# Kernel optimization log

Measured on AMD Instinct MI355X. Metric: run time of the kernel, lower is better.

## Reference

```python
import jax, jax.numpy as jnp
import numpy as np

D = 1024
H = 16
T_BLOCK = 2048


def setup_inputs() -> dict:
    key = jax.random.key(0)
    ks = jax.random.split(key, 12)
    B, T = 2, 2048
    s = lambda k, shape: jax.random.normal(k, shape, jnp.float32) * 0.02
    return {
        "x": jax.random.normal(ks[0], (B, T, D), jnp.float32),
        # layernorms
        "ln1_g": jnp.ones((D,), jnp.float32), "ln1_b": jnp.zeros((D,), jnp.float32),
        "ln2_g": jnp.ones((D,), jnp.float32), "ln2_b": jnp.zeros((D,), jnp.float32),
        # attention qkv projection ([in,out] layout) and output proj
        "w_qkv": s(ks[1], (D, 3 * D)), "b_qkv": jnp.zeros((3 * D,), jnp.float32),
        "w_o": s(ks[2], (D, D)), "b_o": jnp.zeros((D,), jnp.float32),
        # MLP
        "w_fc1": s(ks[3], (D, 4 * D)), "b_fc1": jnp.zeros((4 * D,), jnp.float32),
        "w_fc2": s(ks[4], (4 * D, D)), "b_fc2": jnp.zeros((D,), jnp.float32),
    }


def _layernorm(x, g, b, eps=1e-5):
    mu = jnp.mean(x, axis=-1, keepdims=True)
    var = jnp.var(x, axis=-1, keepdims=True)
    return (x - mu) * jax.lax.rsqrt(var + eps) * g + b


def _attention(x, w_qkv, b_qkv, w_o, b_o):
    B, T, C = x.shape
    hd = C // H
    qkv = x @ w_qkv + b_qkv                      # [B,T,3C]
    q, k, v = jnp.split(qkv, 3, axis=-1)
    split = lambda t: t.reshape(B, T, H, hd).transpose(0, 2, 1, 3)  # [B,H,T,hd]
    q, k, v = split(q), split(k), split(v)
    att = jnp.einsum("bhqd,bhkd->bhqk", q, k) / jnp.sqrt(jnp.float32(hd))
    causal = jnp.tril(jnp.ones((T, T), bool))
    att = jnp.where(causal[None, None], att, -jnp.inf)
    att = jax.nn.softmax(att, axis=-1)
    y = jnp.einsum("bhqk,bhkd->bhqd", att, v)    # [B,H,T,hd]
    y = y.transpose(0, 2, 1, 3).reshape(B, T, C)
    return y @ w_o + b_o


def reference(x, ln1_g, ln1_b, ln2_g, ln2_b, w_qkv, b_qkv, w_o, b_o,
              w_fc1, b_fc1, w_fc2, b_fc2):
    # dropout is identity in eval mode
    x = x + _attention(_layernorm(x, ln1_g, ln1_b), w_qkv, b_qkv, w_o, b_o)
    h = jax.nn.gelu(_layernorm(x, ln2_g, ln2_b) @ w_fc1 + b_fc1)
    return x + (h @ w_fc2 + b_fc2)
```

## Files before the change

kernel.cpp:

```cpp
#include <hip/hip_runtime.h>
#include <hip/hip_bf16.h>


using bf16 = __bf16;
using bf16x8 = __attribute__((ext_vector_type(8))) __bf16;
using floatx4 = __attribute__((ext_vector_type(4))) float;

#define D_ 1024
#define T_ 2048
#define B_ 2
#define H_ 16

static __device__ __forceinline__ bf16 f2bf(float f) { return (bf16)f; }

static __device__ __forceinline__ void async16(const void* g, void* l) {
  __builtin_amdgcn_global_load_lds(
      (const __attribute__((address_space(1))) void*)g,
      (__attribute__((address_space(3))) void*)l, 16, 0, 0);
}

static __device__ __forceinline__ float gelu_f(float v) {
  const float u2 = 1.5957691216057308f * (v + 0.044715f * v * v * v);
  return v / (1.0f + __expf(-u2));
}

__global__ void transpose_cast(const float* __restrict__ in, bf16* __restrict__ out,
                               int K, int N) {
  __shared__ float tile[32][33];
  const int n0 = blockIdx.x * 32, k0 = blockIdx.y * 32;
  const int tx = threadIdx.x, ty = threadIdx.y;
  for (int i = 0; i < 32; i += 8)
    tile[ty + i][tx] = in[(size_t)(k0 + ty + i) * N + n0 + tx];
  __syncthreads();
  for (int i = 0; i < 32; i += 8)
    out[(size_t)(n0 + ty + i) * K + k0 + tx] = f2bf(tile[tx][ty + i]);
}

__global__ __launch_bounds__(256)
void ln_kernel(const float* __restrict__ x, const float* __restrict__ g,
               const float* __restrict__ bsh, bf16* __restrict__ out) {
  const int row = blockIdx.x, tid = threadIdx.x;
  const float4 v = ((const float4*)(x + (size_t)row * D_))[tid];
  float s = v.x + v.y + v.z + v.w;
  float s2 = v.x * v.x + v.y * v.y + v.z * v.z + v.w * v.w;
  for (int off = 32; off; off >>= 1) {
    s += __shfl_xor(s, off);
    s2 += __shfl_xor(s2, off);
  }
  __shared__ float red[8];
  const int wave = tid >> 6, lane = tid & 63;
  if (lane == 0) { red[wave] = s; red[wave + 4] = s2; }
  __syncthreads();
  s = red[0] + red[1] + red[2] + red[3];
  s2 = red[4] + red[5] + red[6] + red[7];
  const float mu = s * (1.0f / D_);
  const float rstd = rsqrtf(s2 * (1.0f / D_) - mu * mu + 1e-5f);
  const float4 gv = ((const float4*)g)[tid];
  const float4 bv = ((const float4*)bsh)[tid];
  bf16 o[4] __attribute__((aligned(8)));
  o[0] = f2bf((v.x - mu) * rstd * gv.x + bv.x);
  o[1] = f2bf((v.y - mu) * rstd * gv.y + bv.y);
  o[2] = f2bf((v.z - mu) * rstd * gv.z + bv.z);
  o[3] = f2bf((v.w - mu) * rstd * gv.w + bv.w);
  *(ushort4*)(out + (size_t)row * D_ + tid * 4) = *(const ushort4*)o;
}

template <int EPI>
__global__ __launch_bounds__(256)
void gemm_bt(const bf16* __restrict__ A, const bf16* __restrict__ Bt,
             const float* __restrict__ bias, const float* __restrict__ res,
             void* __restrict__ Cout, int M, int N, int K) {
  __shared__ __align__(16) bf16 As[128][64];
  __shared__ __align__(16) bf16 Bs[128][64];
  const int tid = threadIdx.x;
  const int wave = tid >> 6, lane = tid & 63;
  const int quad = lane >> 4, l16 = lane & 15;
  const int wr = wave >> 1, wc = wave & 1;
  const int bm = blockIdx.x * 128, bn = blockIdx.y * 128;
  const int lrow8 = lane >> 3;
  const int lcol = (((lane & 7) ^ lrow8) * 8);

  floatx4 acc[4][4] = {};

  for (int k0 = 0; k0 < K; k0 += 64) {
    __syncthreads();
    for (int c = 0; c < 4; c++) {
      const int r = wave * 32 + c * 8;
      async16(&A[(size_t)(bm + r + lrow8) * K + k0 + lcol], &As[r][0]);
      async16(&Bt[(size_t)(bn + r + lrow8) * K + k0 + lcol], &Bs[r][0]);
    }
    __syncthreads();
    for (int ks = 0; ks < 2; ks++) {
      const int fc = ((quad + ks * 4) ^ (l16 & 7)) * 8;
      bf16x8 af[4], bfr[4];
      for (int mt = 0; mt < 4; mt++)
        af[mt] = *(const bf16x8*)&As[wr * 64 + mt * 16 + l16][fc];
      for (int nt = 0; nt < 4; nt++)
        bfr[nt] = *(const bf16x8*)&Bs[wc * 64 + nt * 16 + l16][fc];
      for (int mt = 0; mt < 4; mt++)
        for (int nt = 0; nt < 4; nt++)
          acc[mt][nt] = __builtin_amdgcn_mfma_f32_16x16x32_bf16(
              af[mt], bfr[nt], acc[mt][nt], 0, 0, 0);
    }
  }

  for (int mt = 0; mt < 4; mt++) {
    for (int nt = 0; nt < 4; nt++) {
      const int col = bn + wc * 64 + nt * 16 + l16;
      const float bcol = bias[col];
      for (int i = 0; i < 4; i++) {
        const int row = bm + wr * 64 + mt * 16 + quad * 4 + i;
        float v = acc[mt][nt][i] + bcol;
        if (EPI == 0) {
          ((bf16*)Cout)[(size_t)row * N + col] = f2bf(v);
        } else if (EPI == 1) {
          ((bf16*)Cout)[(size_t)row * N + col] = f2bf(gelu_f(v));
        } else {
          ((float*)Cout)[(size_t)row * N + col] = v + res[(size_t)row * N + col];
        }
      }
    }
  }
}

template <int EPI>
__global__ __launch_bounds__(256)
void gemm64_k64(const bf16* __restrict__ A, const bf16* __restrict__ Bt,
                const float* __restrict__ bias, const float* __restrict__ res,
                void* __restrict__ Cout, int M, int N, int K) {
  __shared__ __align__(16) bf16 As[64][64];
  __shared__ __align__(16) bf16 Bs[128][64];
  const int tid = threadIdx.x;
  const int wave = tid >> 6, lane = tid & 63;
  const int quad = lane >> 4, l16 = lane & 15;
  const int wr = wave >> 1, wc = wave & 1;
  const int bm = blockIdx.x * 64, bn = blockIdx.y * 128;
  const int lrow8 = lane >> 3;
  const int lcol = (((lane & 7) ^ lrow8) * 8);

  floatx4 acc[2][4] = {};

  for (int k0 = 0; k0 < K; k0 += 64) {
    __syncthreads();
    for (int c = 0; c < 2; c++) {
      const int r = wave * 16 + c * 8;
      async16(&A[(size_t)(bm + r + lrow8) * K + k0 + lcol], &As[r][0]);
    }
    for (int c = 0; c < 4; c++) {
      const int r = wave * 32 + c * 8;
      async16(&Bt[(size_t)(bn + r + lrow8) * K + k0 + lcol], &Bs[r][0]);
    }
    __syncthreads();
    for (int ks = 0; ks < 2; ks++) {
      const int fc = ((quad + ks * 4) ^ (l16 & 7)) * 8;
      bf16x8 af[2], bfr[4];
      for (int mt = 0; mt < 2; mt++)
        af[mt] = *(const bf16x8*)&As[wr * 32 + mt * 16 + l16][fc];
      for (int nt = 0; nt < 4; nt++)
        bfr[nt] = *(const bf16x8*)&Bs[wc * 64 + nt * 16 + l16][fc];
      for (int mt = 0; mt < 2; mt++)
        for (int nt = 0; nt < 4; nt++)
          acc[mt][nt] = __builtin_amdgcn_mfma_f32_16x16x32_bf16(
              af[mt], bfr[nt], acc[mt][nt], 0, 0, 0);
    }
  }

  for (int mt = 0; mt < 2; mt++) {
    for (int nt = 0; nt < 4; nt++) {
      const int col = bn + wc * 64 + nt * 16 + l16;
      const float bcol = bias[col];
      for (int i = 0; i < 4; i++) {
        const int row = bm + wr * 32 + mt * 16 + quad * 4 + i;
        float v = acc[mt][nt][i] + bcol;
        if (EPI == 0) {
          ((bf16*)Cout)[(size_t)row * N + col] = f2bf(v);
        } else if (EPI == 1) {
          ((bf16*)Cout)[(size_t)row * N + col] = f2bf(gelu_f(v));
        } else {
          ((float*)Cout)[(size_t)row * N + col] = v + res[(size_t)row * N + col];
        }
      }
    }
  }
}

__global__ __launch_bounds__(256)
void attn_kernel(const bf16* __restrict__ qkv, bf16* __restrict__ y) {
  const int bh = blockIdx.y, b = bh >> 4, h = bh & 15;
  const int tile = (blockIdx.y & 16) ? (int)blockIdx.x : (15 - (int)blockIdx.x);
  const int q0 = tile * 128;
  const int tid = threadIdx.x, wave = tid >> 6, lane = tid & 63;
  const int quad = lane >> 4, l16 = lane & 15;
  const int w32 = wave * 32;

  constexpr int PAD = 80;
  __shared__ __align__(16) bf16 Ks[64][PAD];
  __shared__ __align__(16) bf16 Vts[64][PAD];
  __shared__ __align__(16) bf16 Ps[128][PAD];

  const size_t bbase = (size_t)b * T_ * 3072 + (size_t)h * 64;
  const bf16* Qg = qkv + bbase;
  const bf16* Kg = qkv + bbase + 1024;
  const bf16* Vg = qkv + bbase + 2048;

  bf16x8 ones;
  for (int j = 0; j < 8; j++) ones[j] = f2bf(1.0f);

  const int kr0 = tid >> 3, kc0 = (tid & 7) * 8;
  const int kr1 = (tid + 256) >> 3;

  bf16x8 qf[2][2];
  for (int mt = 0; mt < 2; mt++)
    for (int ks = 0; ks < 2; ks++) {
      bf16x8 t = *(const bf16x8*)
          &Qg[(size_t)(q0 + w32 + mt * 16 + l16) * 3072 + ks * 32 + quad * 8];
      for (int j = 0; j < 8; j++) t[j] = f2bf((float)t[j] * 0.125f);
      qf[mt][ks] = t;
    }

  int4 kreg0 = *(const int4*)&Kg[(size_t)kr0 * 3072 + kc0];
  int4 kreg1 = *(const int4*)&Kg[(size_t)kr1 * 3072 + kc0];
  bf16x8 vreg[2];
  for (int i = 0; i < 2; i++)
    vreg[i] = *(const bf16x8*)&Vg[(size_t)lane * 3072 + (wave + i * 4) * 8];

  floatx4 accY[2][4] = {};
  floatx4 accL[2] = {};

  const int kend = q0 + 64;
  for (int kc = 0; kc <= kend; kc += 64) {
    __syncthreads();
    *(int4*)&Ks[kr0][kc0] = kreg0;
    *(int4*)&Ks[kr1][kc0] = kreg1;
    for (int i = 0; i < 2; i++) {
      const int dc = wave + i * 4;
      for (int j = 0; j < 8; j++) Vts[dc * 8 + j][lane] = vreg[i][j];
    }
    __syncthreads();

    if (kc < kend) {
      kreg0 = *(const int4*)&Kg[(size_t)(kc + 64 + kr0) * 3072 + kc0];
      kreg1 = *(const int4*)&Kg[(size_t)(kc + 64 + kr1) * 3072 + kc0];
      for (int i = 0; i < 2; i++)
        vreg[i] = *(const bf16x8*)
            &Vg[(size_t)(kc + 64 + lane) * 3072 + (wave + i * 4) * 8];
    }

    floatx4 s[2][4];
    for (int nt = 0; nt < 4; nt++) {
      bf16x8 kf0 = *(const bf16x8*)&Ks[nt * 16 + l16][quad * 8];
      bf16x8 kf1 = *(const bf16x8*)&Ks[nt * 16 + l16][32 + quad * 8];
      for (int mt = 0; mt < 2; mt++) {
        floatx4 t = {};
        t = __builtin_amdgcn_mfma_f32_16x16x32_bf16(qf[mt][0], kf0, t, 0, 0, 0);
        t = __builtin_amdgcn_mfma_f32_16x16x32_bf16(qf[mt][1], kf1, t, 0, 0, 0);
        s[mt][nt] = t;
      }
    }
    for (int mt = 0; mt < 2; mt++)
      if (kc + 64 > q0 + w32 + mt * 16) {
        for (int nt = 0; nt < 4; nt++)
          for (int i = 0; i < 4; i++) {
            const int c = kc + nt * 16 + l16;
            const int r = q0 + w32 + mt * 16 + quad * 4 + i;
            if (c > r) s[mt][nt][i] = -1e30f;
          }
      }

    for (int mt = 0; mt < 2; mt++)
      for (int i = 0; i < 4; i++) {
        bf16* prow = &Ps[w32 + mt * 16 + quad * 4 + i][l16];
        for (int nt = 0; nt < 4; nt++)
          prow[nt * 16] = f2bf(__expf(s[mt][nt][i] - 8.0f));
      }
    __builtin_amdgcn_wave_barrier();

    for (int mt = 0; mt < 2; mt++) {
      for (int ks = 0; ks < 2; ks++) {
        bf16x8 pa = *(const bf16x8*)&Ps[w32 + mt * 16 + l16][ks * 32 + quad * 8];
        for (int dt = 0; dt < 4; dt++) {
          bf16x8 vb = *(const bf16x8*)&Vts[dt * 16 + l16][ks * 32 + quad * 8];
          accY[mt][dt] =
              __builtin_amdgcn_mfma_f32_16x16x32_bf16(pa, vb, accY[mt][dt], 0, 0, 0);
        }
        accL[mt] = __builtin_amdgcn_mfma_f32_16x16x32_bf16(pa, ones, accL[mt], 0, 0, 0);
      }
    }
  }

  for (int mt = 0; mt < 2; mt++)
    for (int i = 0; i < 4; i++) {
      const float linv = 1.0f / accL[mt][i];
      const int r = q0 + w32 + mt * 16 + quad * 4 + i;
      for (int dt = 0; dt < 4; dt++)
        y[(size_t)(b * T_ + r) * D_ + h * 64 + dt * 16 + l16] =
            f2bf(accY[mt][dt][i] * linv);
    }
}

extern "C" void kernel_launch(void* const* d_in, const int* in_sizes, int n_in,
                              void* d_out, int out_size, void* d_ws, size_t ws_size,
                              hipStream_t stream) {
  const float* x     = (const float*)d_in[0];
  const float* ln1_g = (const float*)d_in[1];
  const float* ln1_b = (const float*)d_in[2];
  const float* ln2_g = (const float*)d_in[3];
  const float* ln2_b = (const float*)d_in[4];
  const float* w_qkv = (const float*)d_in[5];
  const float* b_qkv = (const float*)d_in[6];
  const float* w_o   = (const float*)d_in[7];
  const float* b_o   = (const float*)d_in[8];
  const float* w_fc1 = (const float*)d_in[9];
  const float* b_fc1 = (const float*)d_in[10];
  const float* w_fc2 = (const float*)d_in[11];
  const float* b_fc2 = (const float*)d_in[12];

  char* p = (char*)d_ws;
  bf16* wqkvT = (bf16*)p; p += (size_t)3072 * 1024 * 2;
  bf16* woT   = (bf16*)p; p += (size_t)1024 * 1024 * 2;
  bf16* wfc1T = (bf16*)p; p += (size_t)4096 * 1024 * 2;
  bf16* wfc2T = (bf16*)p; p += (size_t)1024 * 4096 * 2;
  bf16* ln1   = (bf16*)p; p += (size_t)4096 * 1024 * 2;
  bf16* qkv   = (bf16*)p; p += (size_t)4096 * 3072 * 2;
  bf16* yb    = (bf16*)p; p += (size_t)4096 * 1024 * 2;
  float* x2   = (float*)p; p += (size_t)4096 * 1024 * 4;
  bf16* ln2   = (bf16*)p; p += (size_t)4096 * 1024 * 2;
  bf16* hb    = (bf16*)p; p += (size_t)4096 * 4096 * 2;

  const dim3 tb(32, 8);
  transpose_cast<<<dim3(96, 32), tb, 0, stream>>>(w_qkv, wqkvT, 1024, 3072);
  transpose_cast<<<dim3(32, 32), tb, 0, stream>>>(w_o, woT, 1024, 1024);
  transpose_cast<<<dim3(128, 32), tb, 0, stream>>>(w_fc1, wfc1T, 1024, 4096);
  transpose_cast<<<dim3(32, 128), tb, 0, stream>>>(w_fc2, wfc2T, 4096, 1024);

  ln_kernel<<<4096, 256, 0, stream>>>(x, ln1_g, ln1_b, ln1);
  gemm_bt<0><<<dim3(32, 24), 256, 0, stream>>>(ln1, wqkvT, b_qkv, nullptr, qkv,
                                               4096, 3072, 1024);
  attn_kernel<<<dim3(16, 32), 256, 0, stream>>>(qkv, yb);
  gemm64_k64<2><<<dim3(64, 8), 256, 0, stream>>>(yb, woT, b_o, x, x2,
                                                 4096, 1024, 1024);
  ln_kernel<<<4096, 256, 0, stream>>>(x2, ln2_g, ln2_b, ln2);
  gemm_bt<1><<<dim3(32, 32), 256, 0, stream>>>(ln2, wfc1T, b_fc1, nullptr, hb,
                                               4096, 4096, 1024);
  gemm64_k64<2><<<dim3(64, 8), 256, 0, stream>>>(hb, wfc2T, b_fc2, x2, (float*)d_out,
                                                 4096, 1024, 4096);
}
```

Before: 349.6 us.

## Split K across waves in 64x128 GEMM with LDS reduction

Reworks the 64x128-tile GEMM used for the output projection and FC2 so the four waves split the K dimension in two halves instead of splitting the M rows. Each wave now computes a full 64x64 tile over half of each 64-wide K chunk, and the partial sums are combined through a new float LDS buffer before the epilogue. The aim is more MFMA work per fragment load, since each A and B fragment is reused across four tiles instead of two or four. In exchange it uses more accumulator registers and about 34 KB of extra LDS, which can lower occupancy, and it adds a reduction step with an extra barrier.

After: 362.1 us. +3.6%, slower.

```diff
diff --git a/kernel.cpp b/kernel.cpp
--- a/kernel.cpp
+++ b/kernel.cpp
@@ -125,20 +125,21 @@
 
 template <int EPI>
 __global__ __launch_bounds__(256)
-void gemm64_k64(const bf16* __restrict__ A, const bf16* __restrict__ Bt,
-                const float* __restrict__ bias, const float* __restrict__ res,
-                void* __restrict__ Cout, int M, int N, int K) {
+void gemm_skn(const bf16* __restrict__ A, const bf16* __restrict__ Bt,
+              const float* __restrict__ bias, const float* __restrict__ res,
+              void* __restrict__ Cout, int M, int N, int K) {
   __shared__ __align__(16) bf16 As[64][64];
   __shared__ __align__(16) bf16 Bs[128][64];
+  __shared__ float Sf[2][64][66];
   const int tid = threadIdx.x;
   const int wave = tid >> 6, lane = tid & 63;
   const int quad = lane >> 4, l16 = lane & 15;
-  const int wr = wave >> 1, wc = wave & 1;
+  const int kw = wave >> 1, nw = wave & 1;
   const int bm = blockIdx.x * 64, bn = blockIdx.y * 128;
   const int lrow8 = lane >> 3;
   const int lcol = (((lane & 7) ^ lrow8) * 8);
 
-  floatx4 acc[2][4] = {};
+  floatx4 acc[4][4] = {};
 
   for (int k0 = 0; k0 < K; k0 += 64) {
     __syncthreads();
@@ -151,33 +152,41 @@
       async16(&Bt[(size_t)(bn + r + lrow8) * K + k0 + lcol], &Bs[r][0]);
     }
     __syncthreads();
-    for (int ks = 0; ks < 2; ks++) {
-      const int fc = ((quad + ks * 4) ^ (l16 & 7)) * 8;
-      bf16x8 af[2], bfr[4];
-      for (int mt = 0; mt < 2; mt++)
-        af[mt] = *(const bf16x8*)&As[wr * 32 + mt * 16 + l16][fc];
+    const int fc = ((quad + kw * 4) ^ (l16 & 7)) * 8;
+    bf16x8 af[4], bfr[4];
+    for (int mt = 0; mt < 4; mt++)
+      af[mt] = *(const bf16x8*)&As[mt * 16 + l16][fc];
+    for (int nt = 0; nt < 4; nt++)
+      bfr[nt] = *(const bf16x8*)&Bs[nw * 64 + nt * 16 + l16][fc];
+    for (int mt = 0; mt < 4; mt++)
       for (int nt = 0; nt < 4; nt++)
-        bfr[nt] = *(const bf16x8*)&Bs[wc * 64 + nt * 16 + l16][fc];
-      for (int mt = 0; mt < 2; mt++)
-        for (int nt = 0; nt < 4; nt++)
-          acc[mt][nt] = __builtin_amdgcn_mfma_f32_16x16x32_bf16(
-              af[mt], bfr[nt], acc[mt][nt], 0, 0, 0);
-    }
-  }
-
-  for (int mt = 0; mt < 2; mt++) {
-    for (int nt = 0; nt < 4; nt++) {
-      const int col = bn + wc * 64 + nt * 16 + l16;
-      const float bcol = bias[col];
-      for (int i = 0; i < 4; i++) {
-        const int row = bm + wr * 32 + mt * 16 + quad * 4 + i;
-        float v = acc[mt][nt][i] + bcol;
-        if (EPI == 0) {
-          ((bf16*)Cout)[(size_t)row * N + col] = f2bf(v);
-        } else if (EPI == 1) {
-          ((bf16*)Cout)[(size_t)row * N + col] = f2bf(gelu_f(v));
-        } else {
-          ((float*)Cout)[(size_t)row * N + col] = v + res[(size_t)row * N + col];
+        acc[mt][nt] = __builtin_amdgcn_mfma_f32_16x16x32_bf16(
+            af[mt], bfr[nt], acc[mt][nt], 0, 0, 0);
+  }
+
+  if (kw == 1) {
+    for (int mt = 0; mt < 4; mt++)
+      for (int nt = 0; nt < 4; nt++)
+        for (int i = 0; i < 4; i++)
+          Sf[nw][mt * 16 + quad * 4 + i][nt * 16 + l16] = acc[mt][nt][i];
+  }
+  __syncthreads();
+  if (kw == 0) {
+    for (int mt = 0; mt < 4; mt++) {
+      for (int nt = 0; nt < 4; nt++) {
+        const int col = bn + nw * 64 + nt * 16 + l16;
+        const float bcol = bias[col];
+        for (int i = 0; i < 4; i++) {
+          const int row = bm + mt * 16 + quad * 4 + i;
+          float v = acc[mt][nt][i] +
+                    Sf[nw][mt * 16 + quad * 4 + i][nt * 16 + l16] + bcol;
+          if (EPI == 0) {
+            ((bf16*)Cout)[(size_t)row * N + col] = f2bf(v);
+          } else if (EPI == 1) {
+            ((bf16*)Cout)[(size_t)row * N + col] = f2bf(gelu_f(v));
+          } else {
+            ((float*)Cout)[(size_t)row * N + col] = v + res[(size_t)row * N + col];
+          }
         }
       }
     }
@@ -337,11 +346,11 @@
   gemm_bt<0><<<dim3(32, 24), 256, 0, stream>>>(ln1, wqkvT, b_qkv, nullptr, qkv,
                                                4096, 3072, 1024);
   attn_kernel<<<dim3(16, 32), 256, 0, stream>>>(qkv, yb);
-  gemm64_k64<2><<<dim3(64, 8), 256, 0, stream>>>(yb, woT, b_o, x, x2,
-                                                 4096, 1024, 1024);
+  gemm_skn<2><<<dim3(64, 8), 256, 0, stream>>>(yb, woT, b_o, x, x2,
+                                               4096, 1024, 1024);
   ln_kernel<<<4096, 256, 0, stream>>>(x2, ln2_g, ln2_b, ln2);
   gemm_bt<1><<<dim3(32, 32), 256, 0, stream>>>(ln2, wfc1T, b_fc1, nullptr, hb,
                                                4096, 4096, 1024);
-  gemm64_k64<2><<<dim3(64, 8), 256, 0, stream>>>(hb, wfc2T, b_fc2, x2, (float*)d_out,
-                                                 4096, 1024, 4096);
-}
+  gemm_skn<2><<<dim3(64, 8), 256, 0, stream>>>(hb, wfc2T, b_fc2, x2, (float*)d_out,
+                                               4096, 1024, 4096);
+}
```
